# Kernel tuning notes

Measured on AMD Instinct MI355X. Metric: run time of the kernel, lower is better.

Reference implementation:

```python
import jax, jax.numpy as jnp
import numpy as np

KE_CONST = 14.3996
NUM_GRAPHS = 48
LONG_RANGE_SCALE = 1.0
SQRT2 = 1.41421356  # literal used in the torch jit script


def setup_inputs() -> dict:
    key = jax.random.key(0)
    ks = jax.random.split(key, 10)
    N, F = 6144, 128
    h0 = jax.random.normal(ks[0], (N, F), dtype=jnp.float32)
    h1 = jax.random.normal(ks[1], (N, F), dtype=jnp.float32)
    pos = jax.random.uniform(ks[2], (N, 3), dtype=jnp.float32) * 10.0  # atoms in a ~10A box
    batch = jnp.sort(jax.random.randint(ks[3], (N,), 0, NUM_GRAPHS))
    # q_proj params: Linear(F,F) + SiLU + Linear(F,1,bias=False), init normal(0,0.2)
    q_W1 = jax.random.normal(ks[4], (F, F), dtype=jnp.float32) * 0.2
    q_b1 = jnp.zeros((F,), dtype=jnp.float32)
    q_W2 = jax.random.normal(ks[5], (F, 1), dtype=jnp.float32) * 0.2
    sigma = jnp.asarray(1.0, dtype=jnp.float32)
    # vdw_proj params: Linear(F,F) + SiLU + Linear(F,2)
    s = 1.0 / np.sqrt(F)
    v_W1 = jax.random.normal(ks[6], (F, F), dtype=jnp.float32) * s
    v_b1 = jnp.zeros((F,), dtype=jnp.float32)
    v_W2 = jax.random.normal(ks[7], (F, 2), dtype=jnp.float32) * s
    v_b2 = jnp.zeros((2,), dtype=jnp.float32)
    return {"h0": h0, "h1": h1, "pos": pos, "q_W1": q_W1, "q_b1": q_b1,
            "q_W2": q_W2, "sigma": sigma, "v_W1": v_W1, "v_b1": v_b1,
            "v_W2": v_W2, "v_b2": v_b2, "batch": batch}


def _forward(h0, pos, q_W1, q_b1, q_W2, sigma, v_W1, v_b1, v_W2, v_b2, batch):
    N = h0.shape[0]
    dt = h0.dtype
    # --- charge head: q = Linear(SiLU(Linear(h0))) , per-graph mean-centered ---
    q = jax.nn.silu(h0 @ q_W1 + q_b1) @ q_W2  # [N,1]
    q_sum = jax.ops.segment_sum(q, batch, num_segments=NUM_GRAPHS)  # [G,1]
    counts = jax.ops.segment_sum(jnp.ones((N, 1), dt), batch, num_segments=NUM_GRAPHS)
    q_mean = q_sum / jnp.clip(counts, 1.0)
    q = q - q_mean[batch]
    # --- vdW head: c6, r_vdw = softplus(Linear(SiLU(Linear(h0)))) ---
    vdw_params = jax.nn.silu(h0 @ v_W1 + v_b1) @ v_W2 + v_b2  # [N,2]
    c6 = jax.nn.softplus(vdw_params[:, 0:1])     # [N,1]
    r_vdw = jax.nn.softplus(vdw_params[:, 1:2])  # [N,1]
    # --- dense pairwise geometry (non-periodic branch: cell is None) ---
    diff = pos[:, None, :] - pos[None, :, :]        # [N,N,3]
    dist_sq = jnp.sum(diff * diff, axis=-1)          # [N,N]
    dist = jnp.sqrt(dist_sq + 1e-8)
    batch_mask = batch[:, None] == batch[None, :]
    diag = jnp.eye(N, dtype=bool)
    mask = (batch_mask & ~diag).astype(dt)           # [N,N]
    # --- erf-shielded direct electrostatics ---
    qq = q @ q.T                                     # [N,N]
    shielding = jax.scipy.special.erf(dist / (SQRT2 * sigma))
    e_elec = 0.5 * KE_CONST * jnp.sum(qq * (1.0 / (dist + 1e-8)) * shielding * mask)
    # --- BJ-damped vdW ---
    c6_ij = jnp.sqrt(c6 @ c6.T)
    rvdw_ij = jnp.sqrt(r_vdw @ r_vdw.T)
    damping = dist_sq ** 3 + rvdw_ij ** 6
    e_vdw = 0.5 * jnp.sum(-(c6_ij / (damping + 1e-8)) * mask)
    return (e_elec + e_vdw) * LONG_RANGE_SCALE


def reference(h0, h1, pos, q_W1, q_b1, q_W2, sigma, v_W1, v_b1, v_W2, v_b2, batch):
    # h1 is accepted by the torch forward signature but unused on this path
    return _forward(h0, pos, q_W1, q_b1, q_W2, sigma, v_W1, v_b1, v_W2, v_b2, batch)
```

## Files before the change

### kernel.cpp

```cpp
#include <hip/hip_runtime.h>
#include <math.h>

#define NUM_GRAPHS 48
#define F 128
#define MB 16
#define R 8
#define NPB (NUM_GRAPHS * R)
#define CHUNK 512

__device__ __forceinline__ float softplus_f(float x) {
    return fmaxf(x, 0.0f) + log1pf(expf(-fabsf(x)));
}
__device__ __forceinline__ float silu_f(float x) {
    return x / (1.0f + expf(-x));
}

__global__ __launch_bounds__(256) void mlp_kernel(
    const float* __restrict__ h0,
    const float* __restrict__ qW1, const float* __restrict__ qb1,
    const float* __restrict__ qW2,
    const float* __restrict__ vW1, const float* __restrict__ vb1,
    const float* __restrict__ vW2, const float* __restrict__ vb2,
    const int* __restrict__ batch, int* __restrict__ seg,
    float* __restrict__ q_raw, float* __restrict__ c6s, float* __restrict__ rv3,
    int N)
{
    __shared__ float h0s[MB][F];
    __shared__ float red[4][8][3];
    const int tid = threadIdx.x;
    const int a0 = blockIdx.x * MB;

    if (blockIdx.x == 0) {
        for (int i = tid; i < N; i += 256) {
            int b = batch[i];
            int prev = (i == 0) ? -1 : batch[i - 1];
            for (int g = prev + 1; g <= b; ++g) seg[g] = i;
            if (i == N - 1) {
                for (int g = b + 1; g <= NUM_GRAPHS; ++g) seg[g] = N;
            }
        }
    }

    for (int idx = tid; idx < MB * (F / 4); idx += 256) {
        int a = idx >> 5;
        int kq = idx & 31;
        int row = a0 + a;
        float4 v = make_float4(0.f, 0.f, 0.f, 0.f);
        if (row < N) v = ((const float4*)(h0 + (size_t)row * F))[kq];
        ((float4*)&h0s[a][0])[kq] = v;
    }
    __syncthreads();

    const int j  = tid & 127;
    const int g2 = tid >> 7;

    float accq[8], accv[8];
    const float qb = qb1[j], vb = vb1[j];
    #pragma unroll
    for (int a = 0; a < 8; ++a) { accq[a] = qb; accv[a] = vb; }

    const float* __restrict__ qc = qW1 + j;
    const float* __restrict__ vc = vW1 + j;

    float wq[4], wv[4];
    #pragma unroll
    for (int u = 0; u < 4; ++u) {
        wq[u] = qc[(size_t)u * F];
        wv[u] = vc[(size_t)u * F];
    }

    #pragma unroll 2
    for (int k4 = 0; k4 < F / 4; ++k4) {
        int kn = (k4 < F / 4 - 1) ? (k4 + 1) : k4;
        float nq[4], nv[4];
        #pragma unroll
        for (int u = 0; u < 4; ++u) {
            nq[u] = qc[(size_t)(kn * 4 + u) * F];
            nv[u] = vc[(size_t)(kn * 4 + u) * F];
        }
        #pragma unroll
        for (int a = 0; a < 8; ++a) {
            float4 hv = ((const float4*)&h0s[g2 * 8 + a][0])[k4];
            float tq = accq[a];
            tq = fmaf(hv.x, wq[0], tq);
            tq = fmaf(hv.y, wq[1], tq);
            tq = fmaf(hv.z, wq[2], tq);
            tq = fmaf(hv.w, wq[3], tq);
            accq[a] = tq;
            float tv = accv[a];
            tv = fmaf(hv.x, wv[0], tv);
            tv = fmaf(hv.y, wv[1], tv);
            tv = fmaf(hv.z, wv[2], tv);
            tv = fmaf(hv.w, wv[3], tv);
            accv[a] = tv;
        }
        #pragma unroll
        for (int u = 0; u < 4; ++u) { wq[u] = nq[u]; wv[u] = nv[u]; }
    }

    const float w2q = qW2[j];
    const float w20 = vW2[2 * j];
    const float w21 = vW2[2 * j + 1];
    const int wave = tid >> 6;

    #pragma unroll
    for (int a = 0; a < 8; ++a) {
        float pq = silu_f(accq[a]) * w2q;
        float sv = silu_f(accv[a]);
        float p0 = sv * w20;
        float p1 = sv * w21;
        #pragma unroll
        for (int d = 32; d >= 1; d >>= 1) {
            pq += __shfl_xor(pq, d);
            p0 += __shfl_xor(p0, d);
            p1 += __shfl_xor(p1, d);
        }
        if ((tid & 63) == 0) {
            red[wave][a][0] = pq;
            red[wave][a][1] = p0;
            red[wave][a][2] = p1;
        }
    }
    __syncthreads();

    if (tid < MB) {
        int g  = tid >> 3;
        int al = tid & 7;
        int row = a0 + tid;
        if (row < N) {
            float pq = red[2 * g][al][0] + red[2 * g + 1][al][0];
            float p0 = red[2 * g][al][1] + red[2 * g + 1][al][1];
            float p1 = red[2 * g][al][2] + red[2 * g + 1][al][2];
            q_raw[row] = pq;
            c6s[row] = sqrtf(softplus_f(p0 + vb2[0]));
            float r  = softplus_f(p1 + vb2[1]);
            rv3[row] = r * r * r;
        }
    }
}

__global__ __launch_bounds__(256) void pair_kernel(
    const float* __restrict__ pos,
    const float* __restrict__ q_raw,
    const float* __restrict__ c6s, const float* __restrict__ rv3,
    const int* __restrict__ seg, const float* __restrict__ sigma_p,
    float* __restrict__ part)
{
    __shared__ float xs[CHUNK], ys[CHUNK], zs[CHUNK];
    __shared__ float qs[CHUNK], ss[CHUNK], r3[CHUNK];
    __shared__ float wred[4];

    const int g     = blockIdx.x / R;
    const int slice = blockIdx.x % R;
    const int tid   = threadIdx.x;
    const int wave  = tid >> 6;
    const int lane  = tid & 63;
    const int s0 = seg[g], s1 = seg[g + 1];
    const int n = s1 - s0;

    float acc = 0.0f;
    if (n > 1) {
        float ms = 0.f;
        for (int i = s0 + lane; i < s1; i += 64) ms += q_raw[i];
        #pragma unroll
        for (int d = 32; d >= 1; d >>= 1) ms += __shfl_xor(ms, d);
        const float mean = ms / (float)n;
        const float inv_ss = 1.0f / (1.41421356f * sigma_p[0]);
        const int wv = slice * 4 + wave;

        for (int c0 = s0; c0 < s1; c0 += CHUNK) {
            const int cn = min(CHUNK, s1 - c0);
            __syncthreads();
            for (int idx = tid; idx < cn; idx += 256) {
                int a = c0 + idx;
                xs[idx] = pos[3 * a + 0];
                ys[idx] = pos[3 * a + 1];
                zs[idx] = pos[3 * a + 2];
                qs[idx] = q_raw[a] - mean;
                ss[idx] = c6s[a];
                r3[idx] = rv3[a];
            }
            __syncthreads();

            for (int i = s0 + wv; i < s1; i += 4 * R) {
                float xi = pos[3 * i + 0], yi = pos[3 * i + 1], zi = pos[3 * i + 2];
                float qi = q_raw[i] - mean;
                float si = c6s[i];
                float ri = rv3[i];
                for (int jd = lane; jd < cn; jd += 64) {
                    if (c0 + jd == i) continue;
                    float dx = xi - xs[jd];
                    float dy = yi - ys[jd];
                    float dz = zi - zs[jd];
                    float d2 = fmaf(dx, dx, fmaf(dy, dy, dz * dz));
                    float dist = sqrtf(d2 + 1e-8f);
                    float e1 = qi * qs[jd] * erff(dist * inv_ss) / (dist + 1e-8f);
                    float damp = fmaf(d2 * d2, d2, fmaf(ri, r3[jd], 1e-8f));
                    float e2 = si * ss[jd] / damp;
                    acc += (0.5f * 14.3996f) * e1 - 0.5f * e2;
                }
            }
        }
    }
    #pragma unroll
    for (int d = 32; d >= 1; d >>= 1) acc += __shfl_xor(acc, d);
    if (n > 1) {
        if (lane == 0) wred[wave] = acc;
        __syncthreads();
        if (tid == 0) part[blockIdx.x] = wred[0] + wred[1] + wred[2] + wred[3];
    } else if (tid == 0) {
        part[blockIdx.x] = 0.0f;
    }
}

__global__ __launch_bounds__(256) void finalize_kernel(
    const float* __restrict__ part, int nparts, float* __restrict__ out)
{
    __shared__ double reds[4];
    int tid = threadIdx.x;
    double s = 0.0;
    for (int i = tid; i < nparts; i += 256) s += (double)part[i];
    #pragma unroll
    for (int d = 32; d >= 1; d >>= 1) s += __shfl_xor(s, d);
    if ((tid & 63) == 0) reds[tid >> 6] = s;
    __syncthreads();
    if (tid == 0) out[0] = (float)(reds[0] + reds[1] + reds[2] + reds[3]);
}

extern "C" void kernel_launch(void* const* d_in, const int* in_sizes, int n_in,
                              void* d_out, int out_size, void* d_ws, size_t ws_size,
                              hipStream_t stream) {
    const float* h0   = (const float*)d_in[0];
    const float* pos  = (const float*)d_in[2];
    const float* qW1  = (const float*)d_in[3];
    const float* qb1  = (const float*)d_in[4];
    const float* qW2  = (const float*)d_in[5];
    const float* sig  = (const float*)d_in[6];
    const float* vW1  = (const float*)d_in[7];
    const float* vb1  = (const float*)d_in[8];
    const float* vW2  = (const float*)d_in[9];
    const float* vb2  = (const float*)d_in[10];
    const int*  batch = (const int*)d_in[11];
    const int N = in_sizes[0] / F;

    char* ws = (char*)d_ws;
    int*   seg   = (int*)ws;
    float* part  = (float*)(ws + 256);
    float* q_raw = (float*)(ws + 256 + NPB * 4);
    float* c6s   = q_raw + N;
    float* rv3   = c6s + N;
    float* out   = (float*)d_out;

    mlp_kernel<<<(N + MB - 1) / MB, 256, 0, stream>>>(
        h0, qW1, qb1, qW2, vW1, vb1, vW2, vb2, batch, seg, q_raw, c6s, rv3, N);
    pair_kernel<<<NPB, 256, 0, stream>>>(pos, q_raw, c6s, rv3, seg, sig, part);
    finalize_kernel<<<1, 256, 0, stream>>>(part, NPB, out);
}
```

Before: 110.1 us.

## Fuse MLP, pair, and finalize kernels into one cooperative kernel with grid syncs

Merges the three separate launches into a single cooperative kernel that uses grid-wide syncs between the MLP stage, the pairwise energy stage, and the final reduction, to cut launch overhead and inter-kernel gaps. It also folds the 0.5*KE and 0.5 constants into the shared-memory staged j-values so the inner loop does fewer multiplies. In exchange, every block carries the shared memory of both stages, which lowers occupancy, and grid.sync adds its own barrier cost. The cooperative launch requires all 384 blocks to be co-resident.

```diff
diff --git a/kernel.cpp b/kernel.cpp
--- a/kernel.cpp
+++ b/kernel.cpp
@@ -1,5 +1,8 @@
 #include <hip/hip_runtime.h>
+#include <hip/hip_cooperative_groups.h>
 #include <math.h>
+
+namespace cg = cooperative_groups;
 
 #define NUM_GRAPHS 48
 #define F 128
@@ -15,216 +18,220 @@
     return x / (1.0f + expf(-x));
 }
 
-__global__ __launch_bounds__(256) void mlp_kernel(
+__global__ __launch_bounds__(256) void fused_kernel(
     const float* __restrict__ h0,
     const float* __restrict__ qW1, const float* __restrict__ qb1,
     const float* __restrict__ qW2,
     const float* __restrict__ vW1, const float* __restrict__ vb1,
     const float* __restrict__ vW2, const float* __restrict__ vb2,
-    const int* __restrict__ batch, int* __restrict__ seg,
+    const float* __restrict__ pos, const float* __restrict__ sigma_p,
+    const int* __restrict__ batch,
+    int* __restrict__ seg, float* __restrict__ part,
     float* __restrict__ q_raw, float* __restrict__ c6s, float* __restrict__ rv3,
-    int N)
+    float* __restrict__ out, int N)
 {
+    cg::grid_group grid = cg::this_grid();
+
     __shared__ float h0s[MB][F];
     __shared__ float red[4][8][3];
-    const int tid = threadIdx.x;
-    const int a0 = blockIdx.x * MB;
-
-    if (blockIdx.x == 0) {
-        for (int i = tid; i < N; i += 256) {
-            int b = batch[i];
-            int prev = (i == 0) ? -1 : batch[i - 1];
-            for (int g = prev + 1; g <= b; ++g) seg[g] = i;
-            if (i == N - 1) {
-                for (int g = b + 1; g <= NUM_GRAPHS; ++g) seg[g] = N;
-            }
-        }
-    }
-
-    for (int idx = tid; idx < MB * (F / 4); idx += 256) {
-        int a = idx >> 5;
-        int kq = idx & 31;
-        int row = a0 + a;
-        float4 v = make_float4(0.f, 0.f, 0.f, 0.f);
-        if (row < N) v = ((const float4*)(h0 + (size_t)row * F))[kq];
-        ((float4*)&h0s[a][0])[kq] = v;
-    }
-    __syncthreads();
-
-    const int j  = tid & 127;
-    const int g2 = tid >> 7;
-
-    float accq[8], accv[8];
-    const float qb = qb1[j], vb = vb1[j];
-    #pragma unroll
-    for (int a = 0; a < 8; ++a) { accq[a] = qb; accv[a] = vb; }
-
-    const float* __restrict__ qc = qW1 + j;
-    const float* __restrict__ vc = vW1 + j;
-
-    float wq[4], wv[4];
-    #pragma unroll
-    for (int u = 0; u < 4; ++u) {
-        wq[u] = qc[(size_t)u * F];
-        wv[u] = vc[(size_t)u * F];
-    }
-
-    #pragma unroll 2
-    for (int k4 = 0; k4 < F / 4; ++k4) {
-        int kn = (k4 < F / 4 - 1) ? (k4 + 1) : k4;
-        float nq[4], nv[4];
-        #pragma unroll
-        for (int u = 0; u < 4; ++u) {
-            nq[u] = qc[(size_t)(kn * 4 + u) * F];
-            nv[u] = vc[(size_t)(kn * 4 + u) * F];
-        }
-        #pragma unroll
-        for (int a = 0; a < 8; ++a) {
-            float4 hv = ((const float4*)&h0s[g2 * 8 + a][0])[k4];
-            float tq = accq[a];
-            tq = fmaf(hv.x, wq[0], tq);
-            tq = fmaf(hv.y, wq[1], tq);
-            tq = fmaf(hv.z, wq[2], tq);
-            tq = fmaf(hv.w, wq[3], tq);
-            accq[a] = tq;
-            float tv = accv[a];
-            tv = fmaf(hv.x, wv[0], tv);
-            tv = fmaf(hv.y, wv[1], tv);
-            tv = fmaf(hv.z, wv[2], tv);
-            tv = fmaf(hv.w, wv[3], tv);
-            accv[a] = tv;
-        }
-        #pragma unroll
-        for (int u = 0; u < 4; ++u) { wq[u] = nq[u]; wv[u] = nv[u]; }
-    }
-
-    const float w2q = qW2[j];
-    const float w20 = vW2[2 * j];
-    const float w21 = vW2[2 * j + 1];
-    const int wave = tid >> 6;
-
-    #pragma unroll
-    for (int a = 0; a < 8; ++a) {
-        float pq = silu_f(accq[a]) * w2q;
-        float sv = silu_f(accv[a]);
-        float p0 = sv * w20;
-        float p1 = sv * w21;
-        #pragma unroll
-        for (int d = 32; d >= 1; d >>= 1) {
-            pq += __shfl_xor(pq, d);
-            p0 += __shfl_xor(p0, d);
-            p1 += __shfl_xor(p1, d);
-        }
-        if ((tid & 63) == 0) {
-            red[wave][a][0] = pq;
-            red[wave][a][1] = p0;
-            red[wave][a][2] = p1;
-        }
-    }
-    __syncthreads();
-
-    if (tid < MB) {
-        int g  = tid >> 3;
-        int al = tid & 7;
-        int row = a0 + tid;
-        if (row < N) {
-            float pq = red[2 * g][al][0] + red[2 * g + 1][al][0];
-            float p0 = red[2 * g][al][1] + red[2 * g + 1][al][1];
-            float p1 = red[2 * g][al][2] + red[2 * g + 1][al][2];
-            q_raw[row] = pq;
-            c6s[row] = sqrtf(softplus_f(p0 + vb2[0]));
-            float r  = softplus_f(p1 + vb2[1]);
-            rv3[row] = r * r * r;
-        }
-    }
-}
-
-__global__ __launch_bounds__(256) void pair_kernel(
-    const float* __restrict__ pos,
-    const float* __restrict__ q_raw,
-    const float* __restrict__ c6s, const float* __restrict__ rv3,
-    const int* __restrict__ seg, const float* __restrict__ sigma_p,
-    float* __restrict__ part)
-{
     __shared__ float xs[CHUNK], ys[CHUNK], zs[CHUNK];
     __shared__ float qs[CHUNK], ss[CHUNK], r3[CHUNK];
     __shared__ float wred[4];
 
-    const int g     = blockIdx.x / R;
-    const int slice = blockIdx.x % R;
-    const int tid   = threadIdx.x;
-    const int wave  = tid >> 6;
-    const int lane  = tid & 63;
-    const int s0 = seg[g], s1 = seg[g + 1];
-    const int n = s1 - s0;
-
-    float acc = 0.0f;
-    if (n > 1) {
-        float ms = 0.f;
-        for (int i = s0 + lane; i < s1; i += 64) ms += q_raw[i];
+    const int tid = threadIdx.x;
+    const int bid = blockIdx.x;
+
+    {
+        const int a0 = bid * MB;
+
+        if (bid == 0) {
+            for (int i = tid; i < N; i += 256) {
+                int b = batch[i];
+                int prev = (i == 0) ? -1 : batch[i - 1];
+                for (int g = prev + 1; g <= b; ++g) seg[g] = i;
+                if (i == N - 1) {
+                    for (int g = b + 1; g <= NUM_GRAPHS; ++g) seg[g] = N;
+                }
+            }
+        }
+
+        if (a0 < N) {
+            for (int idx = tid; idx < MB * (F / 4); idx += 256) {
+                int a = idx >> 5;
+                int kq = idx & 31;
+                int row = a0 + a;
+                float4 v = make_float4(0.f, 0.f, 0.f, 0.f);
+                if (row < N) v = ((const float4*)(h0 + (size_t)row * F))[kq];
+                ((float4*)&h0s[a][0])[kq] = v;
+            }
+            __syncthreads();
+
+            const int j  = tid & 127;
+            const int g2 = tid >> 7;
+
+            float accq[8], accv[8];
+            const float qb = qb1[j], vb = vb1[j];
+            #pragma unroll
+            for (int a = 0; a < 8; ++a) { accq[a] = qb; accv[a] = vb; }
+
+            const float* __restrict__ qc = qW1 + j;
+            const float* __restrict__ vc = vW1 + j;
+
+            float wq[4], wv[4];
+            #pragma unroll
+            for (int u = 0; u < 4; ++u) {
+                wq[u] = qc[(size_t)u * F];
+                wv[u] = vc[(size_t)u * F];
+            }
+
+            #pragma unroll 2
+            for (int k4 = 0; k4 < F / 4; ++k4) {
+                int kn = (k4 < F / 4 - 1) ? (k4 + 1) : k4;
+                float nq[4], nv[4];
+                #pragma unroll
+                for (int u = 0; u < 4; ++u) {
+                    nq[u] = qc[(size_t)(kn * 4 + u) * F];
+                    nv[u] = vc[(size_t)(kn * 4 + u) * F];
+                }
+                #pragma unroll
+                for (int a = 0; a < 8; ++a) {
+                    float4 hv = ((const float4*)&h0s[g2 * 8 + a][0])[k4];
+                    float tq = accq[a];
+                    tq = fmaf(hv.x, wq[0], tq);
+                    tq = fmaf(hv.y, wq[1], tq);
+                    tq = fmaf(hv.z, wq[2], tq);
+                    tq = fmaf(hv.w, wq[3], tq);
+                    accq[a] = tq;
+                    float tv = accv[a];
+                    tv = fmaf(hv.x, wv[0], tv);
+                    tv = fmaf(hv.y, wv[1], tv);
+                    tv = fmaf(hv.z, wv[2], tv);
+                    tv = fmaf(hv.w, wv[3], tv);
+                    accv[a] = tv;
+                }
+                #pragma unroll
+                for (int u = 0; u < 4; ++u) { wq[u] = nq[u]; wv[u] = nv[u]; }
+            }
+
+            const float w2q = qW2[j];
+            const float w20 = vW2[2 * j];
+            const float w21 = vW2[2 * j + 1];
+            const int wave = tid >> 6;
+
+            #pragma unroll
+            for (int a = 0; a < 8; ++a) {
+                float pq = silu_f(accq[a]) * w2q;
+                float sv = silu_f(accv[a]);
+                float p0 = sv * w20;
+                float p1 = sv * w21;
+                #pragma unroll
+                for (int d = 32; d >= 1; d >>= 1) {
+                    pq += __shfl_xor(pq, d);
+                    p0 += __shfl_xor(p0, d);
+                    p1 += __shfl_xor(p1, d);
+                }
+                if ((tid & 63) == 0) {
+                    red[wave][a][0] = pq;
+                    red[wave][a][1] = p0;
+                    red[wave][a][2] = p1;
+                }
+            }
+            __syncthreads();
+
+            if (tid < MB) {
+                int gg = tid >> 3;
+                int al = tid & 7;
+                int row = a0 + tid;
+                if (row < N) {
+                    float pq = red[2 * gg][al][0] + red[2 * gg + 1][al][0];
+                    float p0 = red[2 * gg][al][1] + red[2 * gg + 1][al][1];
+                    float p1 = red[2 * gg][al][2] + red[2 * gg + 1][al][2];
+                    q_raw[row] = pq;
+                    c6s[row] = sqrtf(softplus_f(p0 + vb2[0]));
+                    float r  = softplus_f(p1 + vb2[1]);
+                    rv3[row] = r * r * r;
+                }
+            }
+        }
+    }
+
+    grid.sync();
+
+    if (bid < NPB) {
+        const int g     = bid / R;
+        const int slice = bid % R;
+        const int wave  = tid >> 6;
+        const int lane  = tid & 63;
+        const int s0 = seg[g], s1 = seg[g + 1];
+        const int n = s1 - s0;
+
+        float acc = 0.0f;
+        if (n > 1) {
+            float ms = 0.f;
+            for (int i = s0 + lane; i < s1; i += 64) ms += q_raw[i];
+            #pragma unroll
+            for (int d = 32; d >= 1; d >>= 1) ms += __shfl_xor(ms, d);
+            const float mean = ms / (float)n;
+            const float inv_ss = 1.0f / (1.41421356f * sigma_p[0]);
+            const int wv = slice * 4 + wave;
+
+            for (int c0 = s0; c0 < s1; c0 += CHUNK) {
+                const int cn = min(CHUNK, s1 - c0);
+                __syncthreads();
+                for (int idx = tid; idx < cn; idx += 256) {
+                    int a = c0 + idx;
+                    xs[idx] = pos[3 * a + 0];
+                    ys[idx] = pos[3 * a + 1];
+                    zs[idx] = pos[3 * a + 2];
+                    qs[idx] = (q_raw[a] - mean) * (0.5f * 14.3996f);
+                    ss[idx] = c6s[a] * 0.5f;
+                    r3[idx] = rv3[a];
+                }
+                __syncthreads();
+
+                for (int i = s0 + wv; i < s1; i += 4 * R) {
+                    float xi = pos[3 * i + 0], yi = pos[3 * i + 1], zi = pos[3 * i + 2];
+                    float qi = q_raw[i] - mean;
+                    float si = c6s[i];
+                    float ri = rv3[i];
+                    for (int jd = lane; jd < cn; jd += 64) {
+                        if (c0 + jd == i) continue;
+                        float dx = xi - xs[jd];
+                        float dy = yi - ys[jd];
+                        float dz = zi - zs[jd];
+                        float d2 = fmaf(dx, dx, fmaf(dy, dy, dz * dz));
+                        float dist = sqrtf(d2 + 1e-8f);
+                        float e1 = qi * qs[jd] * erff(dist * inv_ss) / (dist + 1e-8f);
+                        float damp = fmaf(d2 * d2, d2, fmaf(ri, r3[jd], 1e-8f));
+                        float e2 = si * ss[jd] / damp;
+                        acc += e1 - e2;
+                    }
+                }
+            }
+        }
         #pragma unroll
-        for (int d = 32; d >= 1; d >>= 1) ms += __shfl_xor(ms, d);
-        const float mean = ms / (float)n;
-        const float inv_ss = 1.0f / (1.41421356f * sigma_p[0]);
-        const int wv = slice * 4 + wave;
-
-        for (int c0 = s0; c0 < s1; c0 += CHUNK) {
-            const int cn = min(CHUNK, s1 - c0);
+        for (int d = 32; d >= 1; d >>= 1) acc += __shfl_xor(acc, d);
+        if (n > 1) {
+            if (lane == 0) wred[wave] = acc;
             __syncthreads();
-            for (int idx = tid; idx < cn; idx += 256) {
-                int a = c0 + idx;
-                xs[idx] = pos[3 * a + 0];
-                ys[idx] = pos[3 * a + 1];
-                zs[idx] = pos[3 * a + 2];
-                qs[idx] = q_raw[a] - mean;
-                ss[idx] = c6s[a];
-                r3[idx] = rv3[a];
-            }
-            __syncthreads();
-
-            for (int i = s0 + wv; i < s1; i += 4 * R) {
-                float xi = pos[3 * i + 0], yi = pos[3 * i + 1], zi = pos[3 * i + 2];
-                float qi = q_raw[i] - mean;
-                float si = c6s[i];
-                float ri = rv3[i];
-                for (int jd = lane; jd < cn; jd += 64) {
-                    if (c0 + jd == i) continue;
-                    float dx = xi - xs[jd];
-                    float dy = yi - ys[jd];
-                    float dz = zi - zs[jd];
-                    float d2 = fmaf(dx, dx, fmaf(dy, dy, dz * dz));
-                    float dist = sqrtf(d2 + 1e-8f);
-                    float e1 = qi * qs[jd] * erff(dist * inv_ss) / (dist + 1e-8f);
-                    float damp = fmaf(d2 * d2, d2, fmaf(ri, r3[jd], 1e-8f));
-                    float e2 = si * ss[jd] / damp;
-                    acc += (0.5f * 14.3996f) * e1 - 0.5f * e2;
-                }
-            }
+            if (tid == 0) part[bid] = wred[0] + wred[1] + wred[2] + wred[3];
+        } else if (tid == 0) {
+            part[bid] = 0.0f;
         }
     }
-    #pragma unroll
-    for (int d = 32; d >= 1; d >>= 1) acc += __shfl_xor(acc, d);
-    if (n > 1) {
-        if (lane == 0) wred[wave] = acc;
+
+    grid.sync();
+
+    if (bid == 0) {
+        double s = 0.0;
+        for (int i = tid; i < NPB; i += 256) s += (double)part[i];
+        #pragma unroll
+        for (int d = 32; d >= 1; d >>= 1) s += __shfl_xor(s, d);
+        __shared__ double reds[4];
+        if ((tid & 63) == 0) reds[tid >> 6] = s;
         __syncthreads();
-        if (tid == 0) part[blockIdx.x] = wred[0] + wred[1] + wred[2] + wred[3];
-    } else if (tid == 0) {
-        part[blockIdx.x] = 0.0f;
+        if (tid == 0) out[0] = (float)(reds[0] + reds[1] + reds[2] + reds[3]);
     }
-}
-
-__global__ __launch_bounds__(256) void finalize_kernel(
-    const float* __restrict__ part, int nparts, float* __restrict__ out)
-{
-    __shared__ double reds[4];
-    int tid = threadIdx.x;
-    double s = 0.0;
-    for (int i = tid; i < nparts; i += 256) s += (double)part[i];
-    #pragma unroll
-    for (int d = 32; d >= 1; d >>= 1) s += __shfl_xor(s, d);
-    if ((tid & 63) == 0) reds[tid >> 6] = s;
-    __syncthreads();
-    if (tid == 0) out[0] = (float)(reds[0] + reds[1] + reds[2] + reds[3]);
 }
 
 extern "C" void kernel_launch(void* const* d_in, const int* in_sizes, int n_in,
@@ -241,18 +248,26 @@
     const float* vW2  = (const float*)d_in[9];
     const float* vb2  = (const float*)d_in[10];
     const int*  batch = (const int*)d_in[11];
-    const int N = in_sizes[0] / F;
+    int N = in_sizes[0] / F;
 
     char* ws = (char*)d_ws;
     int*   seg   = (int*)ws;
     float* part  = (float*)(ws + 256);
-    float* q_raw = (float*)(ws + 256 + NPB * 4);
+    float* q_raw = (float*)(ws + 2048);
     float* c6s   = q_raw + N;
     float* rv3   = c6s + N;
     float* out   = (float*)d_out;
 
-    mlp_kernel<<<(N + MB - 1) / MB, 256, 0, stream>>>(
-        h0, qW1, qb1, qW2, vW1, vb1, vW2, vb2, batch, seg, q_raw, c6s, rv3, N);
-    pair_kernel<<<NPB, 256, 0, stream>>>(pos, q_raw, c6s, rv3, seg, sig, part);
-    finalize_kernel<<<1, 256, 0, stream>>>(part, NPB, out);
-}
+    int nb = (N + MB - 1) / MB;
+    if (nb < NPB) nb = NPB;
+
+    void* args[] = {
+        (void*)&h0, (void*)&qW1, (void*)&qb1, (void*)&qW2,
+        (void*)&vW1, (void*)&vb1, (void*)&vW2, (void*)&vb2,
+        (void*)&pos, (void*)&sig, (void*)&batch,
+        (void*)&seg, (void*)&part, (void*)&q_raw, (void*)&c6s, (void*)&rv3,
+        (void*)&out, (void*)&N
+    };
+    hipLaunchCooperativeKernel((const void*)fused_kernel,
+                               dim3(nb), dim3(256), args, 0, stream);
+}
```

New measurement: 200.3 us. +81.9%, slower.
